# Kernel tuning notes

Measured on AMD Instinct MI355X. Metric: run time of the kernel, lower is better.

The kernel has to match this reference:

```python
import jax, jax.numpy as jnp
import numpy as np

N = 16000; E = 256000; K = 4000; H = 4; D = 128; CL = 16
NODE_VOCAB = 512; TASK_VOCAB = 128; NEG = 0.2


def _gat_sparse(h_in, src, dst, W, a_s, a_d, b):
    # PyG GATConv, heads=H, concat=False, eval mode (attention dropout off)
    n = h_in.shape[0]
    h = (h_in @ W.T).reshape(n, H, D)                       # [N,H,D]
    e = jax.nn.leaky_relu((h * a_s).sum(-1)[src] + (h * a_d).sum(-1)[dst], NEG)  # [E,H]
    emax = jax.ops.segment_max(e, dst, num_segments=n)
    ex = jnp.exp(e - emax[dst])
    den = jax.ops.segment_sum(ex, dst, num_segments=n)
    alpha = ex / (den[dst] + 1e-16)                         # edge softmax over dst
    out = jax.ops.segment_sum(h[src] * alpha[:, :, None], dst, num_segments=n)
    return out.mean(axis=1) + b                             # mean over heads + bias


def reference(x, edge_index, batch, task, node_emb, task_emb,
              W1, as1, ad1, b1, W2, as2, ad2, b2, W3, as3, ad3, b3,
              sag_wrel, sag_brel, sag_wroot, dmon_w, dmon_b,
              Wt, att_s_t, att_d_t, bt, gate_w, gate_b, trans_w, trans_b,
              task_w, task_b, fuse_w, fuse_b, out_w, out_b):
    src0, dst0 = edge_index[0], edge_index[1]
    loops = jnp.arange(N, dtype=src0.dtype)                 # GATConv add_self_loops=True
    src = jnp.concatenate([src0, loops]); dst = jnp.concatenate([dst0, loops])
    h = node_emb[x]
    h = jax.nn.relu(_gat_sparse(h, src, dst, W1, as1, ad1, b1))
    h = jax.nn.relu(_gat_sparse(h, src, dst, W2, as2, ad2, b2))
    h = jax.nn.relu(_gat_sparse(h, src, dst, W3, as3, ad3, b3))
    # SAGPooling: GraphConv score (add-aggr) + top-k (single graph, k=K), tanh gating
    agg = jax.ops.segment_sum(h[src0], dst0, num_segments=N)
    score = (agg @ sag_wrel.T + sag_brel + h @ sag_wroot.T)[:, 0]
    vals, perm = jax.lax.top_k(score, K)
    xp = h[perm] * jnp.tanh(vals)[:, None]                  # [K,D]
    # filter_adj + to_dense_adj: dense [K,K] adjacency among kept nodes (adj[src,dst]+=1)
    new_idx = jnp.full((N,), -1, jnp.int32).at[perm].set(jnp.arange(K, dtype=jnp.int32))
    ni, nj = new_idx[src0], new_idx[dst0]
    valid = (ni >= 0) & (nj >= 0)
    adj = jnp.zeros((K + 1, K + 1), xp.dtype).at[
        jnp.where(valid, ni, K), jnp.where(valid, nj, K)].add(1.0)[:K, :K]
    dx, adj = xp[None], adj[None]                           # [1,K,D], [1,K,K]; mask all-true
    # DMoNPooling
    s = jax.nn.softmax(dx @ dmon_w.T + dmon_b, axis=-1)     # [1,K,CL]
    out_x = jax.nn.selu(jnp.einsum('bnc,bnf->bcf', s, dx))  # [1,CL,D]
    out_adj = jnp.einsum('bnc,bnm,bmd->bcd', s, adj, s)     # [1,CL,CL]
    deg = adj.sum(axis=1)[..., None]                        # einsum('ijk->ik'): [1,K,1]
    m = deg.sum(axis=(1, 2)) / 2
    ca = jnp.einsum('bnc,bnl->bcl', s, deg)                 # [1,CL,1]
    cb = jnp.einsum('bln,bnc->blc', jnp.swapaxes(deg, 1, 2), s)  # [1,1,CL]
    spectral = (-jnp.trace(out_adj - ca @ cb / 2 / m[:, None, None], axis1=1, axis2=2) / 2 / m).mean()
    ss = jnp.einsum('bnc,bnd->bcd', s, s)
    i_s = jnp.eye(CL, dtype=ss.dtype)
    ortho = jnp.linalg.norm(ss / jnp.linalg.norm(ss, axis=(1, 2), keepdims=True)
                            - i_s / jnp.sqrt(jnp.asarray(CL, ss.dtype)), axis=(1, 2)).mean()
    cluster = (jnp.linalg.norm(s.sum(axis=1), axis=1) / K * jnp.sqrt(jnp.asarray(CL, ss.dtype)) - 1).mean()
    gp_loss = spectral + ortho + cluster
    out_adj = out_adj * (1.0 - i_s)                         # zero diagonal
    ds = jnp.sqrt(out_adj.sum(axis=2)) + 1e-15              # [1,CL]
    out_adj = out_adj / ds[:, None, :] / ds[:, :, None]
    # DenseGATConv (add_loop=True sets diag to 1; adj only used as a mask)
    hh = (out_x @ Wt.T).reshape(1, CL, H, D)
    al = jax.nn.leaky_relu((hh * att_s_t).sum(-1)[:, None, :, :]
                           + (hh * att_d_t).sum(-1)[:, :, None, :], NEG)  # [1,i,j,H]
    adj_l = out_adj * (1.0 - i_s) + i_s
    al = jnp.where(adj_l[..., None] == 0, -jnp.inf, al)
    al = jax.nn.softmax(al, axis=2)
    dg = jax.nn.relu(jnp.einsum('bijh,bjhd->bihd', al, hh).mean(axis=2) + bt)  # [1,CL,D]
    # gated readout (DenseAggregation)
    gate = jax.nn.softmax((dg @ gate_w.T + gate_b)[..., 0], axis=-1)           # [1,CL]
    ro = jnp.einsum('bn,bnd->bd', gate, dg @ trans_w.T + trans_b)              # [1,D]
    te = jax.nn.relu(task_emb[task] @ task_w.T + task_b)                       # [1,D]
    fuse = jax.nn.relu(jnp.concatenate([ro, te], axis=-1) @ fuse_w.T + fuse_b)
    out = fuse @ out_w.T + out_b                                               # [1,1]
    return out, gp_loss


def setup_inputs() -> dict:
    key = jax.random.key(0)
    ks = iter(jax.random.split(key, 64))
    def nrm(shape, scale=0.05):
        return jax.random.normal(next(ks), shape, jnp.float32) * scale
    inp = {}
    inp['x'] = jax.random.randint(next(ks), (N,), 0, NODE_VOCAB, dtype=jnp.int32)
    src = jax.random.randint(next(ks), (E,), 0, N, dtype=jnp.int32)
    off = jax.random.randint(next(ks), (E,), 1, N, dtype=jnp.int32)
    inp['edge_index'] = jnp.stack([src, (src + off) % N])  # no self-loops
    inp['batch'] = jnp.zeros((N,), jnp.int32)
    inp['task'] = jax.random.randint(next(ks), (1,), 0, TASK_VOCAB, dtype=jnp.int32)
    inp['node_emb'] = nrm((NODE_VOCAB, D), D ** -0.5)
    inp['task_emb'] = nrm((TASK_VOCAB, D), D ** -0.5)
    for i in (1, 2, 3):
        inp[f'W{i}'] = nrm((H * D, D)); inp[f'as{i}'] = nrm((H, D))
        inp[f'ad{i}'] = nrm((H, D)); inp[f'b{i}'] = jnp.zeros((D,), jnp.float32)
    inp['sag_wrel'] = nrm((1, D)); inp['sag_brel'] = jnp.zeros((1,), jnp.float32)
    inp['sag_wroot'] = nrm((1, D))
    inp['dmon_w'] = nrm((CL, D)); inp['dmon_b'] = jnp.zeros((CL,), jnp.float32)
    inp['Wt'] = nrm((H * D, D)); inp['att_s_t'] = nrm((H, D)); inp['att_d_t'] = nrm((H, D))
    inp['bt'] = jnp.zeros((D,), jnp.float32)
    inp['gate_w'] = nrm((1, D)); inp['gate_b'] = jnp.zeros((1,), jnp.float32)
    inp['trans_w'] = nrm((D, D)); inp['trans_b'] = jnp.zeros((D,), jnp.float32)
    inp['task_w'] = nrm((D, D)); inp['task_b'] = jnp.zeros((D,), jnp.float32)
    inp['fuse_w'] = nrm((D, 2 * D)); inp['fuse_b'] = jnp.zeros((D,), jnp.float32)
    inp['out_w'] = nrm((1, D)); inp['out_b'] = jnp.zeros((1,), jnp.float32)
    return inp
```

## Files before the change

kernel.cpp:

```cpp
#include <hip/hip_runtime.h>
#include <hip/hip_bf16.h>
#include <math.h>

constexpr int NN  = 16000;
constexpr int NE  = 256000;
constexpr int NET = NE + NN;
constexpr int NK  = 4000;
constexpr int NCL = 16;

constexpr int A_ADJ    = 0;
constexpr int A_SS     = 256;
constexpr int A_CSUM   = 512;
constexpr int A_V      = 528;
constexpr int A_DEGSUM = 544;
constexpr int A_OUTX   = 560;
constexpr int ACC_FLOATS = 3072;

typedef short sh8 __attribute__((ext_vector_type(8)));
typedef float f32x4 __attribute__((ext_vector_type(4)));

__device__ inline unsigned fkey(float f){
  unsigned u = __float_as_uint(f);
  return (u & 0x80000000u) ? ~u : (u | 0x80000000u);
}
__device__ inline unsigned short f2bf(float f){
  unsigned u = __float_as_uint(f);
  unsigned r = u + 0x7FFFu + ((u>>16)&1u);
  return (unsigned short)(r>>16);
}
__device__ inline float bflo(unsigned v){ return __uint_as_float(v<<16); }
__device__ inline float bfhi(unsigned v){ return __uint_as_float(v & 0xFFFF0000u); }

__global__ __launch_bounds__(256) void k_init(int* cnt, int* node2k, float* tbuf,
                       float* deg, float* acc,
                       const float* __restrict__ dw, unsigned short* __restrict__ dwb,
                       const float* __restrict__ W0, const float* __restrict__ as0, const float* __restrict__ ad0,
                       const float* __restrict__ W1, const float* __restrict__ as1, const float* __restrict__ ad1,
                       const float* __restrict__ W2, const float* __restrict__ as2, const float* __restrict__ ad2,
                       float* __restrict__ usd, unsigned short* __restrict__ Blay){
  int i = blockIdx.x*blockDim.x + threadIdx.x;
  int stride = gridDim.x*blockDim.x;
  for (int j=i; j<NN; j+=stride){ cnt[j]=0; node2k[j]=-1; }
  for (int j=i; j<NK*NCL; j+=stride) tbuf[j]=0.f;
  for (int j=i; j<NK; j+=stride) deg[j]=0.f;
  for (int j=i; j<ACC_FLOATS; j+=stride) acc[j]=0.f;
  int b = blockIdx.x;
  const float* Wl[3] = {W0, W1, W2};
  const float* al_s[3] = {as0, as1, as2};
  const float* al_d[3] = {ad0, ad1, ad2};
  if (b < 96){
    int layer = b>>5;
    const float* W = Wl[layer];
    int idx = (b&31)*256 + threadIdx.x;
    int lane = idx&63, kc = (idx>>6)&15, c = idx>>10;
    int d = c*16 + (lane&15), q = lane>>4;
    sh8 v;
    #pragma unroll
    for (int j=0;j<8;j++){
      int kkg = kc*32 + q*8 + j;
      int h = kkg>>7, k = kkg&127;
      v[j] = (short)f2bf(W[(size_t)(h*128+d)*128 + k]);
    }
    *((sh8*)(Blay + (size_t)layer*65536 + (size_t)idx*8)) = v;
  } else if (b < 99){
    int layer = b-96;
    const float* W = Wl[layer];
    const float* as_ = al_s[layer];
    const float* ad_ = al_d[layer];
    for (int t2 = threadIdx.x; t2 < 512; t2 += 256){
      int h = t2>>7, k = t2&127;
      float ss=0.f, sd=0.f;
      for (int d=0; d<128; d++){
        float w = W[(size_t)(h*128+d)*128 + k];
        ss += as_[h*128+d]*w;
        sd += ad_[h*128+d]*w;
      }
      usd[layer*1024 + t2] = ss;
      usd[layer*1024 + 512 + t2] = sd;
    }
  } else if (b == 99){
    int idx = threadIdx.x;
    int kc = idx>>6, lane = idx&63;
    int c = lane&15, q = lane>>4;
    sh8 v;
    #pragma unroll
    for (int j=0;j<8;j++) v[j] = (short)f2bf(dw[(size_t)c*128 + kc*32 + q*8 + j]);
    ((sh8*)dwb)[idx] = v;
  }
}

__global__ void k_count(const int* __restrict__ ei, int* __restrict__ cnt){
  int e = blockIdx.x*blockDim.x + threadIdx.x;
  if (e >= NET) return;
  int d = (e < NE) ? ei[NE+e] : (e-NE);
  atomicAdd(&cnt[d], 1);
}

__global__ __launch_bounds__(1024) void k_scan(int* cnt, int* ptr, int* fill){
  __shared__ int sums[1024];
  int t = threadIdx.x;
  constexpr int PER = 16;
  int base = t*PER;
  int v[PER];
  int run = 0;
  #pragma unroll
  for (int i=0;i<PER;i++){
    int idx = base+i;
    int c = (idx<NN)? cnt[idx] : 0;
    v[i] = run; run += c;
  }
  sums[t] = run;
  __syncthreads();
  for (int o=1;o<1024;o<<=1){
    int add = (t>=o)? sums[t-o] : 0;
    __syncthreads();
    sums[t] += add;
    __syncthreads();
  }
  int ex = sums[t] - run;
  #pragma unroll
  for (int i=0;i<PER;i++){
    int idx = base+i;
    if (idx<NN){ int p = ex+v[i]; ptr[idx]=p; fill[idx]=p; }
  }
  if (t==1023) ptr[NN]=sums[1023];
}

__global__ void k_fill(const int* __restrict__ ei, int* cur, int* csrc){
  int e = blockIdx.x*blockDim.x + threadIdx.x;
  if (e >= NET) return;
  int s, d;
  if (e < NE){ s = ei[e]; d = ei[NE+e]; } else { s = e-NE; d = e-NE; }
  int pos = atomicAdd(&cur[d], 1);
  csrc[pos] = s;
}

__global__ __launch_bounds__(64) void k_embsum(const int* __restrict__ x,
    const float* __restrict__ emb, const float* __restrict__ usd,
    unsigned short* __restrict__ hbf, float* __restrict__ sum_s,
    float* __restrict__ sum_d){
  int n = blockIdx.x, lane = threadIdx.x;
  int xv = x[n];
  float2 v = *(const float2*)&emb[(size_t)xv*128 + 2*lane];
  *(ushort2*)&hbf[(size_t)n*128 + 2*lane] = (ushort2){f2bf(v.x), f2bf(v.y)};
  float ps[4], pd[4];
  #pragma unroll
  for (int h=0;h<4;h++){
    float2 us = *(const float2*)&usd[h*128 + 2*lane];
    float2 ud = *(const float2*)&usd[512 + h*128 + 2*lane];
    ps[h] = v.x*us.x + v.y*us.y;
    pd[h] = v.x*ud.x + v.y*ud.y;
  }
  #pragma unroll
  for (int o=32;o>0;o>>=1){
    #pragma unroll
    for (int h=0;h<4;h++){ ps[h]+=__shfl_down(ps[h],o); pd[h]+=__shfl_down(pd[h],o); }
  }
  if (lane==0){
    ((float4*)sum_s)[n] = (float4){ps[0],ps[1],ps[2],ps[3]};
    ((float4*)sum_d)[n] = (float4){pd[0],pd[1],pd[2],pd[3]};
  }
}

__global__ __launch_bounds__(64) void k_edgeagg(const int* __restrict__ ptr,
    const int* __restrict__ csrc,
    const float* __restrict__ sum_s, const float* __restrict__ sum_d,
    const unsigned short* __restrict__ hbf, unsigned short* __restrict__ agg){
  __shared__ float alf[64*4];
  __shared__ int   sN[64];
  int n = blockIdx.x; int lane = threadIdx.x;
  int b0 = ptr[n], b1 = ptr[n+1];
  int deg = b1 - b0;
  float4 sd = ((const float4*)sum_d)[n];
  bool act = lane < deg;
  int s0i = -1;
  float vx=-1e30f, vy=-1e30f, vz=-1e30f, vw=-1e30f;
  if (act){
    s0i = csrc[b0+lane];
    float4 ss = ((const float4*)sum_s)[s0i];
    vx = ss.x+sd.x; vx = vx>0.f? vx : 0.2f*vx;
    vy = ss.y+sd.y; vy = vy>0.f? vy : 0.2f*vy;
    vz = ss.z+sd.z; vz = vz>0.f? vz : 0.2f*vz;
    vw = ss.w+sd.w; vw = vw>0.f? vw : 0.2f*vw;
  }
  float mx=vx, my=vy, mz=vz, mw=vw;
  for (int base=64; base<deg; base+=64){
    int j = b0+base+lane;
    if (j<b1){
      float4 ss = ((const float4*)sum_s)[csrc[j]];
      float t0=ss.x+sd.x; t0=t0>0.f?t0:0.2f*t0; mx=fmaxf(mx,t0);
      float t1=ss.y+sd.y; t1=t1>0.f?t1:0.2f*t1; my=fmaxf(my,t1);
      float t2=ss.z+sd.z; t2=t2>0.f?t2:0.2f*t2; mz=fmaxf(mz,t2);
      float t3=ss.w+sd.w; t3=t3>0.f?t3:0.2f*t3; mw=fmaxf(mw,t3);
    }
  }
  #pragma unroll
  for (int o=1;o<64;o<<=1){
    mx=fmaxf(mx,__shfl_xor(mx,o)); my=fmaxf(my,__shfl_xor(my,o));
    mz=fmaxf(mz,__shfl_xor(mz,o)); mw=fmaxf(mw,__shfl_xor(mw,o));
  }
  float dx = act? __expf(vx-mx):0.f, dy = act? __expf(vy-my):0.f;
  float dz = act? __expf(vz-mz):0.f, dw = act? __expf(vw-mw):0.f;
  for (int base=64; base<deg; base+=64){
    int j = b0+base+lane;
    if (j<b1){
      float4 ss = ((const float4*)sum_s)[csrc[j]];
      float t0=ss.x+sd.x; t0=t0>0.f?t0:0.2f*t0; dx+=__expf(t0-mx);
      float t1=ss.y+sd.y; t1=t1>0.f?t1:0.2f*t1; dy+=__expf(t1-my);
      float t2=ss.z+sd.z; t2=t2>0.f?t2:0.2f*t2; dz+=__expf(t2-mz);
      float t3=ss.w+sd.w; t3=t3>0.f?t3:0.2f*t3; dw+=__expf(t3-mw);
    }
  }
  #pragma unroll
  for (int o=1;o<64;o<<=1){
    dx+=__shfl_xor(dx,o); dy+=__shfl_xor(dy,o);
    dz+=__shfl_xor(dz,o); dw+=__shfl_xor(dw,o);
  }
  float scx = 0.25f/(dx+1e-16f), scy = 0.25f/(dy+1e-16f);
  float scz = 0.25f/(dz+1e-16f), scw = 0.25f/(dw+1e-16f);
  float a00=0.f,a01=0.f,a10=0.f,a11=0.f,a20=0.f,a21=0.f,a30=0.f,a31=0.f;
  for (int base=0; base<deg; base+=64){
    if (base){
      __syncthreads();
      int j = b0+base+lane;
      if (j<b1){
        s0i = csrc[j];
        float4 ss = ((const float4*)sum_s)[s0i];
        vx=ss.x+sd.x; vx=vx>0.f?vx:0.2f*vx;
        vy=ss.y+sd.y; vy=vy>0.f?vy:0.2f*vy;
        vz=ss.z+sd.z; vz=vz>0.f?vz:0.2f*vz;
        vw=ss.w+sd.w; vw=vw>0.f?vw:0.2f*vw;
      }
    }
    if (base+lane < deg){
      alf[lane*4+0]=__expf(vx-mx)*scx; alf[lane*4+1]=__expf(vy-my)*scy;
      alf[lane*4+2]=__expf(vz-mz)*scz; alf[lane*4+3]=__expf(vw-mw)*scw;
      sN[lane]=s0i;
    }
    __syncthreads();
    int m = deg-base; if (m>64) m=64;
    int e=0;
    for (; e+4<=m; e+=4){
      int t0=sN[e], t1=sN[e+1], t2=sN[e+2], t3=sN[e+3];
      float4 A0=*(float4*)&alf[e*4],   A1=*(float4*)&alf[e*4+4];
      float4 A2=*(float4*)&alf[e*4+8], A3=*(float4*)&alf[e*4+12];
      unsigned g0=*(const unsigned*)&hbf[(size_t)t0*128+2*lane];
      unsigned g1=*(const unsigned*)&hbf[(size_t)t1*128+2*lane];
      unsigned g2=*(const unsigned*)&hbf[(size_t)t2*128+2*lane];
      unsigned g3=*(const unsigned*)&hbf[(size_t)t3*128+2*lane];
      float p0=bflo(g0), p1=bfhi(g0);
      a00+=A0.x*p0; a01+=A0.x*p1; a10+=A0.y*p0; a11+=A0.y*p1;
      a20+=A0.z*p0; a21+=A0.z*p1; a30+=A0.w*p0; a31+=A0.w*p1;
      p0=bflo(g1); p1=bfhi(g1);
      a00+=A1.x*p0; a01+=A1.x*p1; a10+=A1.y*p0; a11+=A1.y*p1;
      a20+=A1.z*p0; a21+=A1.z*p1; a30+=A1.w*p0; a31+=A1.w*p1;
      p0=bflo(g2); p1=bfhi(g2);
      a00+=A2.x*p0; a01+=A2.x*p1; a10+=A2.y*p0; a11+=A2.y*p1;
      a20+=A2.z*p0; a21+=A2.z*p1; a30+=A2.w*p0; a31+=A2.w*p1;
      p0=bflo(g3); p1=bfhi(g3);
      a00+=A3.x*p0; a01+=A3.x*p1; a10+=A3.y*p0; a11+=A3.y*p1;
      a20+=A3.z*p0; a21+=A3.z*p1; a30+=A3.w*p0; a31+=A3.w*p1;
    }
    for (; e<m; e++){
      int t0=sN[e];
      float4 A0=*(float4*)&alf[e*4];
      unsigned g0=*(const unsigned*)&hbf[(size_t)t0*128+2*lane];
      float p0=bflo(g0), p1=bfhi(g0);
      a00+=A0.x*p0; a01+=A0.x*p1; a10+=A0.y*p0; a11+=A0.y*p1;
      a20+=A0.z*p0; a21+=A0.z*p1; a30+=A0.w*p0; a31+=A0.w*p1;
    }
  }
  unsigned short* o = agg + (size_t)n*512;
  *(ushort2*)&o[      2*lane] = (ushort2){f2bf(a00), f2bf(a01)};
  *(ushort2*)&o[128 + 2*lane] = (ushort2){f2bf(a10), f2bf(a11)};
  *(ushort2*)&o[256 + 2*lane] = (ushort2){f2bf(a20), f2bf(a21)};
  *(ushort2*)&o[384 + 2*lane] = (ushort2){f2bf(a30), f2bf(a31)};
}

__global__ __launch_bounds__(256) void k_gemmb(const unsigned short* __restrict__ A,
      const unsigned short* __restrict__ B, const float* __restrict__ bias,
      float* __restrict__ C, unsigned short* __restrict__ Cb, int writeF32,
      int mode, const float* __restrict__ usdn,
      const float* __restrict__ wrel, const float* __restrict__ wroot,
      float* __restrict__ sum_s, float* __restrict__ sum_d,
      float* __restrict__ pbuf, float* __restrict__ qbuf){
  __shared__ float U[1024];
  int tid = threadIdx.x;
  if (mode==0){
    for (int i=tid;i<1024;i+=256) U[i]=usdn[i];
  } else {
    if (tid<128) U[tid]=wrel[tid];
    else if (tid<256) U[tid]=wroot[tid-128];
  }
  __syncthreads();
  int w = tid>>6, lane = tid&63;
  int m0 = blockIdx.x*64 + w*16;
  int quad = lane>>4, col16 = lane&15;
  int mrow = m0 + col16;
  const sh8* arow = (const sh8*)(A + (size_t)mrow*512 + quad*8);
  sh8 af[16];
  #pragma unroll
  for (int kc=0;kc<16;kc++) af[kc] = arow[kc*4];
  f32x4 acc[8];
  #pragma unroll
  for (int c=0;c<8;c++) acc[c] = (f32x4){0.f,0.f,0.f,0.f};
  const sh8* bp = (const sh8*)B;
  #pragma unroll
  for (int kc=0;kc<16;kc++){
    #pragma unroll
    for (int c=0;c<8;c++){
      sh8 bf = bp[(c*16+kc)*64 + lane];
      acc[c] = __builtin_amdgcn_mfma_f32_16x16x32_bf16(af[kc], bf, acc[c], 0, 0, 0);
    }
  }
  float br[8];
  #pragma unroll
  for (int c=0;c<8;c++) br[c] = bias[c*16+col16];
  #pragma unroll
  for (int r=0;r<4;r++){
    int m = m0 + quad*4 + r;
    float vv[8];
    #pragma unroll
    for (int c=0;c<8;c++){
      vv[c] = fmaxf(acc[c][r] + br[c], 0.f);
      Cb[(size_t)m*128 + c*16+col16] = f2bf(vv[c]);
      if (writeF32) C[(size_t)m*128 + c*16+col16] = vv[c];
    }
    if (mode==0){
      float p0=0,p1=0,p2=0,p3=0,q0=0,q1=0,q2=0,q3=0;
      #pragma unroll
      for (int c=0;c<8;c++){
        int o = c*16+col16;
        float val = vv[c];
        p0+=val*U[o];     p1+=val*U[128+o]; p2+=val*U[256+o]; p3+=val*U[384+o];
        q0+=val*U[512+o]; q1+=val*U[640+o]; q2+=val*U[768+o]; q3+=val*U[896+o];
      }
      #pragma unroll
      for (int o2=1;o2<16;o2<<=1){
        p0+=__shfl_xor(p0,o2); p1+=__shfl_xor(p1,o2); p2+=__shfl_xor(p2,o2); p3+=__shfl_xor(p3,o2);
        q0+=__shfl_xor(q0,o2); q1+=__shfl_xor(q1,o2); q2+=__shfl_xor(q2,o2); q3+=__shfl_xor(q3,o2);
      }
      if (col16==0){
        ((float4*)sum_s)[m] = (float4){p0,p1,p2,p3};
        ((float4*)sum_d)[m] = (float4){q0,q1,q2,q3};
      }
    } else {
      float pp=0.f, qq=0.f;
      #pragma unroll
      for (int c=0;c<8;c++){
        int o = c*16+col16;
        pp += vv[c]*U[o]; qq += vv[c]*U[128+o];
      }
      #pragma unroll
      for (int o2=1;o2<16;o2<<=1){ pp+=__shfl_xor(pp,o2); qq+=__shfl_xor(qq,o2); }
      if (col16==0){ pbuf[m]=pp; qbuf[m]=qq; }
    }
  }
}

__global__ __launch_bounds__(64) void k_sagw(const int* __restrict__ ptr,
                           const int* __restrict__ csrc,
                           const float* __restrict__ p, const float* __restrict__ q,
                           const float* __restrict__ brel, float* __restrict__ score){
  int n = blockIdx.x; int lane = threadIdx.x;
  int b0=ptr[n], b1=ptr[n+1];
  float s=0.f;
  for (int j=b0+lane; j<b1; j+=64){
    int sj=csrc[j];
    if (sj!=n) s+=p[sj];
  }
  #pragma unroll
  for (int o=32;o>0;o>>=1) s += __shfl_down(s,o);
  if (lane==0) score[n] = s + q[n] + brel[0];
}

__global__ __launch_bounds__(1024) void k_topk(const float* __restrict__ score,
                                               int* __restrict__ sel){
  __shared__ int hist[8*257];
  __shared__ int hmerge[256];
  __shared__ unsigned sh_prefix;
  __shared__ int sh_rem;
  __shared__ int cntGT, cntEQ;
  __shared__ int ties[256];
  int t = threadIdx.x;
  int lane = t & 63;
  int rep = t >> 7;
  unsigned keys[16];
  #pragma unroll
  for (int j=0;j<16;j++){
    int i = t + j*1024;
    keys[j] = (i<NN) ? fkey(score[i]) : 0u;
  }
  if (t==0){ sh_prefix=0u; sh_rem=NK; cntGT=0; cntEQ=0; }
  __syncthreads();
  for (int p=0;p<4;p++){
    int shift = 24-8*p;
    for (int i=t;i<8*257;i+=1024) hist[i]=0;
    __syncthreads();
    unsigned prefix = sh_prefix;
    #pragma unroll
    for (int j=0;j<16;j++){
      bool val = (j<15) || (t < (NN - 15*1024));
      unsigned u = keys[j];
      bool ok = val && ((p==0) || ((u>>(shift+8)) == (prefix>>(shift+8))));
      int b = (int)((u>>shift)&255u);
      unsigned long long act = __ballot(ok);
      if (act){
        int leader = (int)(__ffsll((long long)act)-1);
        int bl = __shfl(b, leader);
        unsigned long long same = __ballot(ok && b==bl);
        if (same==act){
          if (lane==leader) atomicAdd(&hist[rep*257+bl], (int)__popcll(act));
        } else if (ok){
          atomicAdd(&hist[rep*257+b], 1);
        }
      }
    }
    __syncthreads();
    if (t<256){
      int v=0;
      #pragma unroll
      for (int r=0;r<8;r++) v += hist[r*257+t];
      hmerge[t]=v;
    }
    __syncthreads();
    if (t<64){
      int l = t;
      int b0 = 4*(63-l);
      int c3 = hmerge[b0+3], c2 = hmerge[b0+2], c1 = hmerge[b0+1], c0 = hmerge[b0];
      int gs = c0+c1+c2+c3;
      int incl = gs;
      #pragma unroll
      for (int o=1;o<64;o<<=1){
        int v = __shfl_up(incl, o);
        if (l>=o) incl += v;
      }
      int excl = incl - gs;
      int rem = sh_rem;
      int rl = rem - excl;
      if (rl > 0 && rl <= gs){
        unsigned pre = sh_prefix;
        if (rl > c3){ rl -= c3;
          if (rl > c2){ rl -= c2;
            if (rl > c1){ rl -= c1;
              sh_prefix = pre | ((unsigned)b0<<shift);     sh_rem = rl;
            } else { sh_prefix = pre | ((unsigned)(b0+1)<<shift); sh_rem = rl; }
          } else { sh_prefix = pre | ((unsigned)(b0+2)<<shift);   sh_rem = rl; }
        } else { sh_prefix = pre | ((unsigned)(b0+3)<<shift);     sh_rem = rl; }
      }
    }
    __syncthreads();
  }
  unsigned Tu = sh_prefix;
  #pragma unroll
  for (int j=0;j<16;j++){
    int i = t + j*1024;
    bool val = (i<NN);
    unsigned u = keys[j];
    bool g = val && (u>Tu), e = val && (u==Tu);
    unsigned long long mg = __ballot(g);
    if (mg){
      int leader = (int)(__ffsll((long long)mg)-1);
      int base = 0;
      if (lane==leader) base = atomicAdd(&cntGT, (int)__popcll(mg));
      base = __shfl(base, leader);
      if (g){
        int pos = base + (int)__popcll(mg & ((1ull<<lane)-1ull));
        sel[pos] = i;
      }
    }
    unsigned long long me = __ballot(e);
    if (me){
      int leader = (int)(__ffsll((long long)me)-1);
      int base = 0;
      if (lane==leader) base = atomicAdd(&cntEQ, (int)__popcll(me));
      base = __shfl(base, leader);
      if (e){
        int pos = base + (int)__popcll(me & ((1ull<<lane)-1ull));
        if (pos<256) ties[pos] = i;
      }
    }
  }
  __syncthreads();
  if (t==0){
    int base=cntGT, rem=sh_rem, nt=min(cntEQ,256);
    for (int r=0;r<rem;r++){
      int best=0x7fffffff, bi=-1;
      for (int q2=0;q2<nt;q2++){ int v=ties[q2]; if (v>=0 && v<best){best=v;bi=q2;} }
      sel[base+r] = (bi>=0)? best : 0;
      if (bi>=0) ties[bi]=-1;
    }
  }
}

__global__ __launch_bounds__(256) void k_gassign(const int* __restrict__ sel,
                          const float* __restrict__ score,
                          const float* __restrict__ h, float* __restrict__ xp,
                          int* __restrict__ node2k,
                          const unsigned short* __restrict__ dwb,
                          const float* __restrict__ db,
                          float* __restrict__ sA){
  __shared__ unsigned short xs[16*128];
  __shared__ int seln[16];
  __shared__ float gs[16];
  int k0 = blockIdx.x*16;
  int t = threadIdx.x;
  if (t<16){
    int n = sel[k0+t];
    seln[t] = n;
    node2k[n] = k0+t;
    gs[t] = tanhf(score[n]);
  }
  __syncthreads();
  #pragma unroll
  for (int it=0; it<8; it++){
    int idx = t + it*256;
    int row = idx>>7, col = idx&127;
    float v = h[(size_t)seln[row]*128 + col]*gs[row];
    xp[(size_t)(k0+row)*128 + col] = v;
    xs[idx] = f2bf(v);
  }
  __syncthreads();
  if (t<64){
    int lane = t;
    int quad = lane>>4, col = lane&15;
    const sh8* ar = (const sh8*)&xs[col*128 + quad*8];
    const sh8* br = (const sh8*)dwb;
    f32x4 acc = (f32x4){0.f,0.f,0.f,0.f};
    #pragma unroll
    for (int kc=0;kc<4;kc++){
      sh8 af = ar[kc*4];
      sh8 bf = br[kc*64 + lane];
      acc = __builtin_amdgcn_mfma_f32_16x16x32_bf16(af, bf, acc, 0, 0, 0);
    }
    float bias = db[col];
    #pragma unroll
    for (int r=0;r<4;r++){
      float lg = acc[r] + bias;
      float mx = lg;
      #pragma unroll
      for (int o=1;o<16;o<<=1) mx = fmaxf(mx, __shfl_xor(mx, o));
      float e = __expf(lg - mx);
      float sm = e;
      #pragma unroll
      for (int o=1;o<16;o<<=1) sm += __shfl_xor(sm, o);
      sA[(size_t)(k0+quad*4+r)*16 + col] = e/sm;
    }
  }
}

__global__ void k_edgepool(const int* __restrict__ ei, const int* __restrict__ node2k,
                           const float* __restrict__ sA, float* __restrict__ tbuf,
                           float* __restrict__ deg){
  int e = blockIdx.x*blockDim.x + threadIdx.x;
  if (e >= NE) return;
  int ni = node2k[ei[e]];
  int nj = node2k[ei[NE+e]];
  if (ni >= 0 && nj >= 0){
    atomicAdd(&deg[nj], 1.f);
    const float* sr = &sA[(size_t)nj*16];
    float* tr = &tbuf[(size_t)ni*16];
    #pragma unroll
    for (int c=0;c<16;c++) atomicAdd(&tr[c], sr[c]);
  }
}

constexpr int P_BLOCKS = 80;
constexpr int P_ROWS   = NK / P_BLOCKS;
constexpr int P_CHUNK  = 25;

__global__ __launch_bounds__(256) void k_pool(const float* __restrict__ sA,
                                              const float* __restrict__ xp,
                                              const float* __restrict__ tb,
                                              const float* __restrict__ deg,
                                              float* __restrict__ acc){
  __shared__ float sv[P_CHUNK*16];
  __shared__ float tv[P_CHUNK*16];
  __shared__ float dv[P_CHUNK];
  __shared__ float xv[P_CHUNK*128];
  int t = threadIdx.x;
  int c = t>>4, d = t&15;
  float loc[8] = {0,0,0,0,0,0,0,0};
  float a_adj=0.f, a_ss=0.f, a_cs=0.f, a_v=0.f, a_dg=0.f;
  int r0 = blockIdx.x*P_ROWS;
  for (int ch=0; ch<P_ROWS; ch+=P_CHUNK){
    int base = r0+ch;
    for (int i=t;i<P_CHUNK*16;i+=256){
      sv[i] = sA[(size_t)(base+(i>>4))*16 + (i&15)];
      tv[i] = tb[(size_t)(base+(i>>4))*16 + (i&15)];
    }
    for (int i=t;i<P_CHUNK*128;i+=256)
      xv[i] = xp[(size_t)(base+(i>>7))*128 + (i&127)];
    if (t<P_CHUNK) dv[t]=deg[base+t];
    __syncthreads();
    for (int r=0;r<P_CHUNK;r++){
      float sc = sv[r*16+c];
      a_adj += sc*tv[r*16+d];
      a_ss  += sc*sv[r*16+d];
      if (d==0){ a_cs += sc; a_v += sc*dv[r]; }
      if (t==0) a_dg += dv[r];
      #pragma unroll
      for (int j=0;j<8;j++){
        int o=t+j*256;
        loc[j] += sv[r*16+(o>>7)]*xv[r*128+(o&127)];
      }
    }
    __syncthreads();
  }
  atomicAdd(&acc[A_ADJ + t], a_adj);
  atomicAdd(&acc[A_SS + t], a_ss);
  if (d==0){ atomicAdd(&acc[A_CSUM+c], a_cs); atomicAdd(&acc[A_V+c], a_v); }
  if (t==0) atomicAdd(&acc[A_DEGSUM], a_dg);
  #pragma unroll
  for (int j=0;j<8;j++) atomicAdd(&acc[A_OUTX + t + j*256], loc[j]);
}

__device__ float block_sum_256(float v, float* red){
  int t = threadIdx.x;
  red[t]=v; __syncthreads();
  #pragma unroll
  for (int o=128;o>0;o>>=1){ if (t<o) red[t]+=red[t+o]; __syncthreads(); }
  float r = red[0]; __syncthreads();
  return r;
}

__global__ __launch_bounds__(256) void k_tail(float* __restrict__ acc,
    const float* __restrict__ Wt,
    const float* __restrict__ att_s, const float* __restrict__ att_d,
    const float* __restrict__ bt, const float* __restrict__ gate_w,
    const float* __restrict__ gate_b, const float* __restrict__ trans_w,
    const float* __restrict__ trans_b, const int* __restrict__ task,
    const float* __restrict__ task_emb, const float* __restrict__ task_w,
    const float* __restrict__ task_b, const float* __restrict__ fuse_w,
    const float* __restrict__ fuse_b, const float* __restrict__ out_w,
    const float* __restrict__ out_b, float* __restrict__ dout){
  __shared__ float red[256];
  __shared__ float dsv[16];
  __shared__ float adjn[256];
  __shared__ float sx[2048];
  __shared__ float hh[8192];
  __shared__ float al[1024];
  __shared__ float asrc[64], adst[64];
  __shared__ float dg[2048];
  __shared__ float gate[16];
  __shared__ float gvec[128];
  __shared__ float ro[128], te[128], fu[128];
  int t = threadIdx.x;
  int c = t>>4, dcol = t&15;
  float m = 0.5f*acc[A_DEGSUM];
  float ssv = acc[A_SS+t];
  float tr    = block_sum_256((t<16)? acc[A_ADJ + t*16 + t] : 0.f, red);
  float sumv2 = block_sum_256((t<16)? acc[A_V+t]*acc[A_V+t] : 0.f, red);
  float ss2   = block_sum_256(ssv*ssv, red);
  float cs2   = block_sum_256((t<16)? acc[A_CSUM+t]*acc[A_CSUM+t] : 0.f, red);
  float ssn = sqrtf(ss2);
  float term = ssv/ssn - ((c==dcol)? 0.25f : 0.f);
  float ortho2 = block_sum_256(term*term, red);
  if (t==0){
    float spectral = -(tr - sumv2/(2.f*m))/(2.f*m);
    float ortho = sqrtf(ortho2);
    float cluster = sqrtf(cs2)/(float)NK*4.f - 1.f;
    dout[1] = spectral + ortho + cluster;
  }
  float z = (c==dcol)? 0.f : acc[A_ADJ+t];
  red[t]=z; __syncthreads();
  for (int o=8;o>0;o>>=1){ if (dcol<o) red[t]+=red[t+o]; __syncthreads(); }
  if (dcol==0) dsv[c]=sqrtf(red[c*16])+1e-15f;
  __syncthreads();
  adjn[t] = z/(dsv[c]*dsv[dcol]);
  #pragma unroll
  for (int j=0;j<8;j++){
    int idx = t + j*256;
    float xv = acc[A_OUTX+idx];
    float s2 = (xv > 0.f)? xv : 1.6732632423543772f*expm1f(xv);
    sx[idx] = 1.0507009873554805f*s2;
  }
  __syncthreads();
  {
    const float4* sx4 = (const float4*)sx;
    for (int o = t; o < 512; o += 256){
      const float4* w4 = (const float4*)(Wt + (size_t)o*128);
      float s[16];
      #pragma unroll
      for (int c2=0;c2<16;c2++) s[c2]=0.f;
      #pragma unroll 8
      for (int k=0;k<32;k++){
        float4 b = w4[k];
        #pragma unroll
        for (int c2=0;c2<16;c2++){
          float4 a = sx4[c2*32 + k];
          s[c2] += a.x*b.x + a.y*b.y + a.z*b.z + a.w*b.w;
        }
      }
      #pragma unroll
      for (int c2=0;c2<16;c2++) hh[c2*512 + o] = s[c2];
    }
  }
  __syncthreads();
  if (t<128){
    int j = t>>3; int h = (t>>1)&3; int w = t&1;
    const float* hr = &hh[j*512 + h*128];
    const float* a = (w? att_d : att_s) + h*128;
    float s=0.f;
    for (int k2=0;k2<128;k2++) s += hr[k2]*a[k2];
    if (w) adst[j*4+h]=s; else asrc[j*4+h]=s;
  }
  __syncthreads();
  for (int idx=t; idx<1024; idx+=256){
    int h = idx&3, j=(idx>>2)&15, i=idx>>6;
    float v = asrc[j*4+h] + adst[i*4+h];
    v = v>0.f? v : 0.2f*v;
    float adjl = (i==j)? 1.f : adjn[i*16+j];
    al[idx] = (adjl==0.f)? -1e30f : v;
  }
  __syncthreads();
  if (t<64){
    int i=t>>2, h=t&3;
    float mx=-1e30f;
    for (int j=0;j<16;j++) mx = fmaxf(mx, al[(i*16+j)*4+h]);
    float sum=0.f;
    for (int j=0;j<16;j++){ float e=__expf(al[(i*16+j)*4+h]-mx); al[(i*16+j)*4+h]=e; sum+=e; }
    float inv = 1.f/sum;
    for (int j=0;j<16;j++) al[(i*16+j)*4+h]*=inv;
  }
  __syncthreads();
  for (int idx=t; idx<2048; idx+=256){
    int i=idx>>7, d=idx&127;
    float s=0.f;
    for (int h=0;h<4;h++)
      for (int j=0;j<16;j++)
        s += al[(i*16+j)*4+h]*hh[j*512+h*128+d];
    dg[idx] = fmaxf(0.25f*s + bt[d], 0.f);
  }
  __syncthreads();
  if (t<16){
    float s=0.f;
    for (int d2=0;d2<128;d2++) s += dg[t*128+d2]*gate_w[d2];
    red[t] = s + gate_b[0];
  }
  __syncthreads();
  if (t<16){
    float mx=-1e30f; for (int i=0;i<16;i++) mx=fmaxf(mx,red[i]);
    float s=0.f; for (int i=0;i<16;i++) s+=__expf(red[i]-mx);
    gate[t]=__expf(red[t]-mx)/s;
  }
  __syncthreads();
  if (t<128){
    float s=0.f;
    for (int i=0;i<16;i++) s += gate[i]*dg[i*128+t];
    gvec[t]=s;
  }
  __syncthreads();
  if (t<128){
    float s=0.f;
    for (int k2=0;k2<128;k2++) s += gvec[k2]*trans_w[t*128+k2];
    ro[t]=s+trans_b[t];
    int tk = task[0];
    float s2=0.f;
    for (int k2=0;k2<128;k2++) s2 += task_emb[(size_t)tk*128+k2]*task_w[t*128+k2];
    te[t]=fmaxf(s2+task_b[t],0.f);
  }
  __syncthreads();
  if (t<128){
    float s=0.f;
    for (int k2=0;k2<128;k2++) s += ro[k2]*fuse_w[t*256+k2] + te[k2]*fuse_w[t*256+128+k2];
    fu[t]=fmaxf(s+fuse_b[t],0.f);
  }
  __syncthreads();
  float v = (t<128)? fu[t]*out_w[t] : 0.f;
  red[t]=v; __syncthreads();
  for (int o=128;o>0;o>>=1){ if (t<o) red[t]+=red[t+o]; __syncthreads(); }
  if (t==0) dout[0]=red[0]+out_b[0];
}

extern "C" void kernel_launch(void* const* d_in, const int* in_sizes, int n_in,
                              void* d_out, int out_size, void* d_ws, size_t ws_size,
                              hipStream_t stream){
  const int* x        = (const int*)d_in[0];
  const int* ei       = (const int*)d_in[1];
  const int* task     = (const int*)d_in[3];
  const float* node_emb = (const float*)d_in[4];
  const float* task_emb = (const float*)d_in[5];
  const float* W[3]  = {(const float*)d_in[6],  (const float*)d_in[10], (const float*)d_in[14]};
  const float* As_[3]= {(const float*)d_in[7],  (const float*)d_in[11], (const float*)d_in[15]};
  const float* Ad_[3]= {(const float*)d_in[8],  (const float*)d_in[12], (const float*)d_in[16]};
  const float* Bb[3] = {(const float*)d_in[9],  (const float*)d_in[13], (const float*)d_in[17]};
  const float* wrel  = (const float*)d_in[18];
  const float* brel  = (const float*)d_in[19];
  const float* wroot = (const float*)d_in[20];
  const float* dmon_w= (const float*)d_in[21];
  const float* dmon_b= (const float*)d_in[22];
  const float* Wt    = (const float*)d_in[23];
  const float* att_s = (const float*)d_in[24];
  const float* att_d = (const float*)d_in[25];
  const float* btb   = (const float*)d_in[26];
  const float* gate_w= (const float*)d_in[27];
  const float* gate_b= (const float*)d_in[28];
  const float* trans_w=(const float*)d_in[29];
  const float* trans_b=(const float*)d_in[30];
  const float* task_w= (const float*)d_in[31];
  const float* task_b= (const float*)d_in[32];
  const float* fuse_w= (const float*)d_in[33];
  const float* fuse_b= (const float*)d_in[34];
  const float* out_w = (const float*)d_in[35];
  const float* out_b = (const float*)d_in[36];
  float* dout = (float*)d_out;
  (void)in_sizes; (void)n_in; (void)out_size; (void)ws_size;

  char* base = (char*)d_ws;
  size_t off = 0;
  auto alloc = [&](size_t bytes)->char*{
    off = (off + 255) & ~(size_t)255;
    char* r = base + off; off += bytes; return r;
  };
  int* csr_ptr  = (int*)alloc((size_t)(NN+1)*4);
  int* csr_fill = (int*)alloc((size_t)NN*4);
  int* csr_src  = (int*)alloc((size_t)NET*4);
  int* sel      = (int*)alloc((size_t)NK*4);
  int* node2k   = (int*)alloc((size_t)NN*4);
  float* score  = (float*)alloc((size_t)NN*4);
  float* pbuf   = (float*)alloc((size_t)NN*4);
  float* qbuf   = (float*)alloc((size_t)NN*4);
  float* h_a    = (float*)alloc((size_t)NN*128*4);
  unsigned short* hbf  = (unsigned short*)alloc((size_t)NN*128*2);
  unsigned short* aggb = (unsigned short*)alloc((size_t)NN*512*2);
  unsigned short* blay = (unsigned short*)alloc((size_t)3*65536*2);
  unsigned short* dwb  = (unsigned short*)alloc((size_t)256*8*2);
  float* usd    = (float*)alloc((size_t)3*1024*4);
  float* sum_s  = (float*)alloc((size_t)NN*4*4);
  float* sum_d  = (float*)alloc((size_t)NN*4*4);
  float* xp     = (float*)alloc((size_t)NK*128*4);
  float* sA     = (float*)alloc((size_t)NK*16*4);
  float* tbuf   = (float*)alloc((size_t)NK*16*4);
  float* deg    = (float*)alloc((size_t)NK*4);
  float* acc    = (float*)alloc((size_t)ACC_FLOATS*4);

  k_init<<<256, 256, 0, stream>>>(csr_fill, node2k, tbuf, deg, acc, dmon_w, dwb,
                                  W[0], As_[0], Ad_[0], W[1], As_[1], Ad_[1],
                                  W[2], As_[2], Ad_[2], usd, blay);
  k_count<<<(NET+255)/256, 256, 0, stream>>>(ei, csr_fill);
  k_scan<<<1, 1024, 0, stream>>>(csr_fill, csr_ptr, csr_fill);
  k_fill<<<(NET+255)/256, 256, 0, stream>>>(ei, csr_fill, csr_src);
  k_embsum<<<NN, 64, 0, stream>>>(x, node_emb, usd, hbf, sum_s, sum_d);

  for (int l=0;l<3;l++){
    k_edgeagg<<<NN, 64, 0, stream>>>(csr_ptr, csr_src, sum_s, sum_d, hbf, aggb);
    if (l<2){
      k_gemmb<<<NN/64, 256, 0, stream>>>(aggb, blay + (size_t)l*65536, Bb[l],
                                         h_a, hbf, 0, 0, usd + (l+1)*1024,
                                         nullptr, nullptr, sum_s, sum_d,
                                         nullptr, nullptr);
    } else {
      k_gemmb<<<NN/64, 256, 0, stream>>>(aggb, blay + (size_t)2*65536, Bb[2],
                                         h_a, hbf, 1, 1, nullptr,
                                         wrel, wroot, nullptr, nullptr,
                                         pbuf, qbuf);
    }
  }
  k_sagw<<<NN, 64, 0, stream>>>(csr_ptr, csr_src, pbuf, qbuf, brel, score);
  k_topk<<<1, 1024, 0, stream>>>(score, sel);
  k_gassign<<<NK/16, 256, 0, stream>>>(sel, score, h_a, xp, node2k, dwb, dmon_b, sA);
  k_edgepool<<<(NE+255)/256, 256, 0, stream>>>(ei, node2k, sA, tbuf, deg);
  k_pool<<<P_BLOCKS, 256, 0, stream>>>(sA, xp, tbuf, deg, acc);
  k_tail<<<1, 256, 0, stream>>>(acc, Wt, att_s, att_d, btb, gate_w, gate_b,
                                trans_w, trans_b, task, task_emb, task_w, task_b,
                                fuse_w, fuse_b, out_w, out_b, dout);
}
```

Baseline: 444.4 us.

## Use bf16 MFMA for tail GAT projection and aggregation, vectorize tail dot products

The single-block tail kernel's 16x128 by 128x512 projection and its attention-weighted aggregation move from scalar fp32 loops to bf16 MFMA 16x16x32 instructions. The Wt weight is pre-swizzled to bf16 in the init kernel using extra blocks. The remaining small dot products in the tail switch to float4 loads. This targets the serial latency of the one-block tail, at the cost of bf16 rounding in those GEMMs and more shared memory.

```diff
diff --git a/kernel.cpp b/kernel.cpp
--- a/kernel.cpp
+++ b/kernel.cpp
@@ -37,6 +37,7 @@
                        const float* __restrict__ W0, const float* __restrict__ as0, const float* __restrict__ ad0,
                        const float* __restrict__ W1, const float* __restrict__ as1, const float* __restrict__ ad1,
                        const float* __restrict__ W2, const float* __restrict__ as2, const float* __restrict__ ad2,
+                       const float* __restrict__ Wt, unsigned short* __restrict__ Wtb,
                        float* __restrict__ usd, unsigned short* __restrict__ Blay){
   int i = blockIdx.x*blockDim.x + threadIdx.x;
   int stride = gridDim.x*blockDim.x;
@@ -86,6 +87,14 @@
     #pragma unroll
     for (int j=0;j<8;j++) v[j] = (short)f2bf(dw[(size_t)c*128 + kc*32 + q*8 + j]);
     ((sh8*)dwb)[idx] = v;
+  } else if (b < 132){
+    int idx = (b-100)*256 + threadIdx.x;
+    int lane = idx&63, kc = (idx>>6)&3, ntile = idx>>8;
+    int o = ntile*16 + (lane&15), q = lane>>4;
+    sh8 v;
+    #pragma unroll
+    for (int j=0;j<8;j++) v[j] = (short)f2bf(Wt[(size_t)o*128 + kc*32 + q*8 + j]);
+    ((sh8*)Wtb)[idx] = v;
   }
 }
 
@@ -625,7 +634,7 @@
 }
 
 __global__ __launch_bounds__(256) void k_tail(float* __restrict__ acc,
-    const float* __restrict__ Wt,
+    const unsigned short* __restrict__ Wtb,
     const float* __restrict__ att_s, const float* __restrict__ att_d,
     const float* __restrict__ bt, const float* __restrict__ gate_w,
     const float* __restrict__ gate_b, const float* __restrict__ trans_w,
@@ -638,8 +647,11 @@
   __shared__ float dsv[16];
   __shared__ float adjn[256];
   __shared__ float sx[2048];
+  __shared__ unsigned short sxb[2048];
   __shared__ float hh[8192];
+  __shared__ unsigned short hhb[8192];
   __shared__ float al[1024];
+  __shared__ unsigned short albf[16*64];
   __shared__ float asrc[64], adst[64];
   __shared__ float dg[2048];
   __shared__ float gate[16];
@@ -673,36 +685,47 @@
     int idx = t + j*256;
     float xv = acc[A_OUTX+idx];
     float s2 = (xv > 0.f)? xv : 1.6732632423543772f*expm1f(xv);
-    sx[idx] = 1.0507009873554805f*s2;
+    float v = 1.0507009873554805f*s2;
+    sx[idx] = v;
+    sxb[idx] = f2bf(v);
   }
   __syncthreads();
   {
-    const float4* sx4 = (const float4*)sx;
-    for (int o = t; o < 512; o += 256){
-      const float4* w4 = (const float4*)(Wt + (size_t)o*128);
-      float s[16];
-      #pragma unroll
-      for (int c2=0;c2<16;c2++) s[c2]=0.f;
-      #pragma unroll 8
-      for (int k=0;k<32;k++){
-        float4 b = w4[k];
-        #pragma unroll
-        for (int c2=0;c2<16;c2++){
-          float4 a = sx4[c2*32 + k];
-          s[c2] += a.x*b.x + a.y*b.y + a.z*b.z + a.w*b.w;
-        }
-      }
-      #pragma unroll
-      for (int c2=0;c2<16;c2++) hh[c2*512 + o] = s[c2];
+    int w = t>>6, lane = t&63;
+    int quad = lane>>4, col = lane&15;
+    sh8 af[4];
+    #pragma unroll
+    for (int kc=0;kc<4;kc++) af[kc] = *(const sh8*)&sxb[col*128 + kc*32 + quad*8];
+    const sh8* bp = (const sh8*)Wtb;
+    #pragma unroll
+    for (int nt2=0; nt2<8; nt2++){
+      int ntile = w*8 + nt2;
+      f32x4 a2 = (f32x4){0.f,0.f,0.f,0.f};
+      #pragma unroll
+      for (int kc=0;kc<4;kc++){
+        sh8 bf = bp[(ntile*4+kc)*64 + lane];
+        a2 = __builtin_amdgcn_mfma_f32_16x16x32_bf16(af[kc], bf, a2, 0, 0, 0);
+      }
+      #pragma unroll
+      for (int r=0;r<4;r++){
+        int mm = quad*4 + r;
+        int oo = ntile*16 + col;
+        hh[mm*512 + oo] = a2[r];
+        hhb[mm*512 + oo] = f2bf(a2[r]);
+      }
     }
   }
   __syncthreads();
   if (t<128){
     int j = t>>3; int h = (t>>1)&3; int w = t&1;
-    const float* hr = &hh[j*512 + h*128];
-    const float* a = (w? att_d : att_s) + h*128;
+    const float4* hr = (const float4*)&hh[j*512 + h*128];
+    const float4* a4 = (const float4*)((w? att_d : att_s) + h*128);
     float s=0.f;
-    for (int k2=0;k2<128;k2++) s += hr[k2]*a[k2];
+    #pragma unroll
+    for (int k2=0;k2<32;k2++){
+      float4 a = hr[k2], b = a4[k2];
+      s += a.x*b.x + a.y*b.y + a.z*b.z + a.w*b.w;
+    }
     if (w) adst[j*4+h]=s; else asrc[j*4+h]=s;
   }
   __syncthreads();
@@ -721,21 +744,52 @@
     float sum=0.f;
     for (int j=0;j<16;j++){ float e=__expf(al[(i*16+j)*4+h]-mx); al[(i*16+j)*4+h]=e; sum+=e; }
     float inv = 1.f/sum;
-    for (int j=0;j<16;j++) al[(i*16+j)*4+h]*=inv;
-  }
-  __syncthreads();
-  for (int idx=t; idx<2048; idx+=256){
-    int i=idx>>7, d=idx&127;
-    float s=0.f;
-    for (int h=0;h<4;h++)
-      for (int j=0;j<16;j++)
-        s += al[(i*16+j)*4+h]*hh[j*512+h*128+d];
-    dg[idx] = fmaxf(0.25f*s + bt[d], 0.f);
+    for (int j=0;j<16;j++){
+      float v = al[(i*16+j)*4+h]*inv;
+      albf[i*64 + h*16 + j] = f2bf(v);
+    }
+  }
+  __syncthreads();
+  {
+    int w = t>>6, lane = t&63;
+    int quad = lane>>4, col = lane&15;
+    sh8 af2[2];
+    #pragma unroll
+    for (int kc=0;kc<2;kc++) af2[kc] = *(const sh8*)&albf[col*64 + kc*32 + quad*8];
+    #pragma unroll
+    for (int nt2=0; nt2<2; nt2++){
+      int ntile = w*2 + nt2;
+      int d = ntile*16 + col;
+      f32x4 a2 = (f32x4){0.f,0.f,0.f,0.f};
+      #pragma unroll
+      for (int kc=0;kc<2;kc++){
+        sh8 bf;
+        #pragma unroll
+        for (int j2=0;j2<8;j2++){
+          int k = kc*32 + quad*8 + j2;
+          int h2 = k>>4, jj = k&15;
+          bf[j2] = (short)hhb[jj*512 + h2*128 + d];
+        }
+        a2 = __builtin_amdgcn_mfma_f32_16x16x32_bf16(af2[kc], bf, a2, 0, 0, 0);
+      }
+      float bd = bt[d];
+      #pragma unroll
+      for (int r=0;r<4;r++){
+        int i = quad*4 + r;
+        dg[i*128 + d] = fmaxf(0.25f*a2[r] + bd, 0.f);
+      }
+    }
   }
   __syncthreads();
   if (t<16){
     float s=0.f;
-    for (int d2=0;d2<128;d2++) s += dg[t*128+d2]*gate_w[d2];
+    const float4* d4 = (const float4*)&dg[t*128];
+    const float4* g4 = (const float4*)gate_w;
+    #pragma unroll
+    for (int k2=0;k2<32;k2++){
+      float4 a = d4[k2], b = g4[k2];
+      s += a.x*b.x + a.y*b.y + a.z*b.z + a.w*b.w;
+    }
     red[t] = s + gate_b[0];
   }
   __syncthreads();
@@ -753,17 +807,41 @@
   __syncthreads();
   if (t<128){
     float s=0.f;
-    for (int k2=0;k2<128;k2++) s += gvec[k2]*trans_w[t*128+k2];
+    const float4* tw = (const float4*)(trans_w + (size_t)t*128);
+    const float4* gv = (const float4*)gvec;
+    #pragma unroll
+    for (int k2=0;k2<32;k2++){
+      float4 a = gv[k2], b = tw[k2];
+      s += a.x*b.x + a.y*b.y + a.z*b.z + a.w*b.w;
+    }
     ro[t]=s+trans_b[t];
     int tk = task[0];
+    const float4* te4 = (const float4*)(task_emb + (size_t)tk*128);
+    const float4* tw2 = (const float4*)(task_w + (size_t)t*128);
     float s2=0.f;
-    for (int k2=0;k2<128;k2++) s2 += task_emb[(size_t)tk*128+k2]*task_w[t*128+k2];
+    #pragma unroll
+    for (int k2=0;k2<32;k2++){
+      float4 a = te4[k2], b = tw2[k2];
+      s2 += a.x*b.x + a.y*b.y + a.z*b.z + a.w*b.w;
+    }
     te[t]=fmaxf(s2+task_b[t],0.f);
   }
   __syncthreads();
   if (t<128){
     float s=0.f;
-    for (int k2=0;k2<128;k2++) s += ro[k2]*fuse_w[t*256+k2] + te[k2]*fuse_w[t*256+128+k2];
+    const float4* fw = (const float4*)(fuse_w + (size_t)t*256);
+    const float4* ro4 = (const float4*)ro;
+    const float4* te4 = (const float4*)te;
+    #pragma unroll
+    for (int k2=0;k2<32;k2++){
+      float4 a = ro4[k2], b = fw[k2];
+      s += a.x*b.x + a.y*b.y + a.z*b.z + a.w*b.w;
+    }
+    #pragma unroll
+    for (int k2=0;k2<32;k2++){
+      float4 a = te4[k2], b = fw[32+k2];
+      s += a.x*b.x + a.y*b.y + a.z*b.z + a.w*b.w;
+    }
     fu[t]=fmaxf(s+fuse_b[t],0.f);
   }
   __syncthreads();
@@ -826,6 +904,7 @@
   unsigned short* aggb = (unsigned short*)alloc((size_t)NN*512*2);
   unsigned short* blay = (unsigned short*)alloc((size_t)3*65536*2);
   unsigned short* dwb  = (unsigned short*)alloc((size_t)256*8*2);
+  unsigned short* wtb  = (unsigned short*)alloc((size_t)65536*2);
   float* usd    = (float*)alloc((size_t)3*1024*4);
   float* sum_s  = (float*)alloc((size_t)NN*4*4);
   float* sum_d  = (float*)alloc((size_t)NN*4*4);
@@ -837,7 +916,7 @@
 
   k_init<<<256, 256, 0, stream>>>(csr_fill, node2k, tbuf, deg, acc, dmon_w, dwb,
                                   W[0], As_[0], Ad_[0], W[1], As_[1], Ad_[1],
-                                  W[2], As_[2], Ad_[2], usd, blay);
+                                  W[2], As_[2], Ad_[2], Wt, wtb, usd, blay);
   k_count<<<(NET+255)/256, 256, 0, stream>>>(ei, csr_fill);
   k_scan<<<1, 1024, 0, stream>>>(csr_fill, csr_ptr, csr_fill);
   k_fill<<<(NET+255)/256, 256, 0, stream>>>(ei, csr_fill, csr_src);
@@ -862,7 +941,7 @@
   k_gassign<<<NK/16, 256, 0, stream>>>(sel, score, h_a, xp, node2k, dwb, dmon_b, sA);
   k_edgepool<<<(NE+255)/256, 256, 0, stream>>>(ei, node2k, sA, tbuf, deg);
   k_pool<<<P_BLOCKS, 256, 0, stream>>>(sA, xp, tbuf, deg, acc);
-  k_tail<<<1, 256, 0, stream>>>(acc, Wt, att_s, att_d, btb, gate_w, gate_b,
+  k_tail<<<1, 256, 0, stream>>>(acc, wtb, att_s, att_d, btb, gate_w, gate_b,
                                 trans_w, trans_b, task, task_emb, task_w, task_b,
                                 fuse_w, fuse_b, out_w, out_b, dout);
 }
```

After: 413.5 us (median of 2 runs). 7.0% less time.
